# Kernel optimization log

Measured on AMD Instinct MI355X. Metric: run time of the kernel, lower is better.

Reference implementation:

```python
import math
import jax, jax.numpy as jnp
import numpy as np

N_HEAD = 16

def setup_inputs() -> dict:
    key = jax.random.key(0)
    ks = jax.random.split(key, 3)
    B, T, C = 2, 2048, 1024
    x = jax.random.normal(ks[0], (B, T, C), dtype=jnp.float32)
    W_attn = jax.random.normal(ks[1], (3 * C, C), dtype=jnp.float32) * (1.0 / math.sqrt(C))
    b_attn = jnp.zeros((3 * C,), dtype=jnp.float32)
    W_proj = jax.random.normal(ks[2], (C, C), dtype=jnp.float32) * (1.0 / math.sqrt(C))
    b_proj = jnp.zeros((C,), dtype=jnp.float32)
    return {"x": x, "W_attn": W_attn, "b_attn": b_attn, "W_proj": W_proj, "b_proj": b_proj}

def reference(x, W_attn, b_attn, W_proj, b_proj):
    B, T, C = x.shape
    H = N_HEAD
    Dh = C // H
    qkv = x @ W_attn.T + b_attn                      # [B,T,3C]
    q, k, v = jnp.split(qkv, 3, axis=-1)
    q = q.reshape(B, T, H, Dh).transpose(0, 2, 1, 3)  # [B,H,T,Dh]
    k = k.reshape(B, T, H, Dh).transpose(0, 2, 1, 3)
    v = v.reshape(B, T, H, Dh).transpose(0, 2, 1, 3)
    att = jnp.einsum('bhqd,bhkd->bhqk', q, k) * (1.0 / math.sqrt(Dh))
    # ALiBi-style RPE: bias[h, r, c] = -(r - c) * 2^(-8/H * (h+1)) for c <= r, 0 above diag
    rows = jnp.arange(T)[:, None]
    cols = jnp.arange(T)[None, :]
    dist = jnp.minimum((cols - rows).astype(jnp.float32), 0.0)  # [T,T]
    slopes = 2.0 ** (-8.0 / H * (jnp.arange(H, dtype=jnp.float32) + 1.0))  # [H]
    att = att + slopes[None, :, None, None] * dist[None, None]
    causal = cols <= rows                              # [T,T]
    att = jnp.where(causal[None, None], att, -jnp.inf)
    att = jax.nn.softmax(att, axis=-1)                 # dropout p=0.0 -> identity
    y = jnp.einsum('bhqk,bhkd->bhqd', att, v)          # [B,H,T,Dh]
    y = y.transpose(0, 2, 1, 3).reshape(B, T, C)
    y = y @ W_proj.T + b_proj
    return y
```

## Files before the change

kernel.cpp:

```cpp
#include <hip/hip_runtime.h>

typedef __bf16 bf16x8 __attribute__((ext_vector_type(8)));
typedef __bf16 bf16x4 __attribute__((ext_vector_type(4)));
typedef float  f32x4  __attribute__((ext_vector_type(4)));
typedef float  f32x16 __attribute__((ext_vector_type(16)));

#define TSEQ 2048
#define CDIM 1024
#define NHEAD 16
#define DH 64
#define SCALE2 0.1803368801111137f

__device__ __forceinline__ void gl_lds16(const void* g, void* l) {
  __builtin_amdgcn_global_load_lds(
      (const __attribute__((address_space(1))) unsigned int*)g,
      (__attribute__((address_space(3))) unsigned int*)l, 16, 0, 0);
}

__device__ __forceinline__ float fexp2(float x) { return __builtin_amdgcn_exp2f(x); }

__device__ __forceinline__ unsigned cvtpk(float a, float b) {
  unsigned r;
  asm("v_cvt_pk_bf16_f32 %0, %1, %2" : "=v"(r) : "v"(a), "v"(b));
  return r;
}
__device__ __forceinline__ void permswap(unsigned& x, unsigned& y) {
  asm("v_permlane32_swap_b32 %0, %1" : "+v"(x), "+v"(y));
}

__device__ __forceinline__ float tsum16(const f32x16& s) {
  float a0 = s[0] + s[1], a1 = s[2] + s[3], a2 = s[4] + s[5], a3 = s[6] + s[7];
  float a4 = s[8] + s[9], a5 = s[10] + s[11], a6 = s[12] + s[13], a7 = s[14] + s[15];
  float b0 = a0 + a1, b1 = a2 + a3, b2 = a4 + a5, b3 = a6 + a7;
  return (b0 + b1) + (b2 + b3);
}

__global__ __launch_bounds__(256) void cvt_bf16_all(
    const float* __restrict__ x, const float* __restrict__ wa,
    const float* __restrict__ wp, __bf16* __restrict__ xb,
    __bf16* __restrict__ wab, __bf16* __restrict__ wpb) {
  int i = blockIdx.x * 256 + threadIdx.x;
  const float* in;
  __bf16* out;
  int off;
  if (i < 524288)      { in = x;  out = xb;  off = i; }
  else if (i < 917504) { in = wa; out = wab; off = i - 524288; }
  else                 { in = wp; out = wpb; off = i - 917504; }
  const float4* p = (const float4*)(in + (size_t)off * 8);
  float4 a = p[0], b = p[1];
  bf16x8 r;
  r[0] = (__bf16)a.x; r[1] = (__bf16)a.y; r[2] = (__bf16)a.z; r[3] = (__bf16)a.w;
  r[4] = (__bf16)b.x; r[5] = (__bf16)b.y; r[6] = (__bf16)b.z; r[7] = (__bf16)b.w;
  *(bf16x8*)(out + (size_t)off * 8) = r;
}

__global__ __launch_bounds__(256) void gemm_qkv(
    const __bf16* __restrict__ A, const __bf16* __restrict__ Bw,
    const float* __restrict__ bias,
    __bf16* __restrict__ q_pack, __bf16* __restrict__ k_pack,
    __bf16* __restrict__ v_pack, int K) {
  __shared__ alignas(16) __bf16 lda[128 * 64];
  __shared__ alignas(16) __bf16 ldb[128 * 64];
  const int tid = threadIdx.x;
  const int lane = tid & 63, wid = tid >> 6;
  const int wm = wid >> 1, wn = wid & 1;
  const int hw = (int)(blockIdx.x + 24 * blockIdx.y);
  const int logi = (hw & 7) * 96 + (hw >> 3);
  const int row0 = (logi / 24) * 128, col0 = (logi % 24) * 128;
  f32x4 acc[4][4] = {};

  const int srow = lane >> 3;
  const int scb = ((lane & 7) ^ (lane >> 3)) * 16;

  for (int k0 = 0; k0 < K; k0 += 64) {
#pragma unroll
    for (int j = 0; j < 4; ++j) {
      int blk = j * 4 + wid;
      int r = blk * 8 + srow;
      char* la = (char*)lda + blk * 1024;
      char* lb = (char*)ldb + blk * 1024;
      gl_lds16((const char*)(A + (size_t)(row0 + r) * K + k0) + scb, la);
      gl_lds16((const char*)(Bw + (size_t)(col0 + r) * K + k0) + scb, lb);
    }
    __syncthreads();
#pragma unroll
    for (int kk = 0; kk < 2; ++kk) {
      const int sl = (((kk << 2) | (lane >> 4)) ^ (lane & 7)) * 16;
      bf16x8 af[4], bfr[4];
#pragma unroll
      for (int m = 0; m < 4; ++m)
        af[m] = *(const bf16x8*)((const char*)lda +
                                 (wm * 64 + m * 16 + (lane & 15)) * 128 + sl);
#pragma unroll
      for (int n = 0; n < 4; ++n)
        bfr[n] = *(const bf16x8*)((const char*)ldb +
                                  (wn * 64 + n * 16 + (lane & 15)) * 128 + sl);
#pragma unroll
      for (int m = 0; m < 4; ++m)
#pragma unroll
        for (int n = 0; n < 4; ++n)
          acc[m][n] = __builtin_amdgcn_mfma_f32_16x16x32_bf16(bfr[n], af[m], acc[m][n], 0, 0, 0);
    }
    __syncthreads();
  }
#pragma unroll
  for (int m = 0; m < 4; ++m) {
    const int r = row0 + wm * 64 + m * 16 + (lane & 15);
    const int bb = r >> 11, t = r & 2047;
    const size_t bhb = (size_t)bb * NHEAD;
#pragma unroll
    for (int n = 0; n < 4; ++n) {
      const int c0 = col0 + wn * 64 + n * 16 + (lane >> 4) * 4;
      const int sec = c0 >> 10;
      const int cc0 = c0 & 1023;
      const int hh = cc0 >> 6, d0 = cc0 & 63;
      const size_t bh = bhb + hh;
      const float4 bv = *(const float4*)&bias[c0];
      const float v0 = acc[m][n][0] + bv.x;
      const float v1 = acc[m][n][1] + bv.y;
      const float v2 = acc[m][n][2] + bv.z;
      const float v3 = acc[m][n][3] + bv.w;
      if (sec == 2) {
        const int j2 = t >> 5, kh = (t >> 4) & 1, half = d0 >> 5;
        const size_t base = (bh * 256 + (size_t)(j2 * 4 + kh * 2 + half)) * 512 + (size_t)(t & 7);
        const int l2v0 = (d0 & 31) + ((t >> 3) & 1) * 32;
        v_pack[base + (size_t)(l2v0 + 0) * 8] = (__bf16)v0;
        v_pack[base + (size_t)(l2v0 + 1) * 8] = (__bf16)v1;
        v_pack[base + (size_t)(l2v0 + 2) * 8] = (__bf16)v2;
        v_pack[base + (size_t)(l2v0 + 3) * 8] = (__bf16)v3;
      } else {
        const int ch = t >> 5, mm = d0 >> 4;
        const int l2 = (t & 31) + ((d0 >> 3) & 1) * 32, e0 = d0 & 7;
        const size_t idx = ((bh * 64 + ch) * 4 + (size_t)mm) * 512 + (size_t)l2 * 8 + e0;
        bf16x4 w;
        if (sec == 0) {
          w[0] = (__bf16)(v0 * SCALE2); w[1] = (__bf16)(v1 * SCALE2);
          w[2] = (__bf16)(v2 * SCALE2); w[3] = (__bf16)(v3 * SCALE2);
          *(bf16x4*)&q_pack[idx] = w;
        } else {
          w[0] = (__bf16)v0; w[1] = (__bf16)v1; w[2] = (__bf16)v2; w[3] = (__bf16)v3;
          *(bf16x4*)&k_pack[idx] = w;
        }
      }
    }
  }
}

__global__ __launch_bounds__(256) void gemm_proj(
    const __bf16* __restrict__ A, const __bf16* __restrict__ Bw,
    const float* __restrict__ bias, float* __restrict__ outf) {
  const int K = CDIM, N = CDIM;
  __shared__ alignas(16) __bf16 lda[64 * 64];
  __shared__ alignas(16) __bf16 ldb[128 * 64];
  const int tid = threadIdx.x;
  const int lane = tid & 63, wid = tid >> 6;
  const int hw = (int)(blockIdx.x + 8 * blockIdx.y);
  const int logi = (hw & 7) * 64 + (hw >> 3);
  const int row0 = (logi / 8) * 64, col0 = (logi % 8) * 128;
  f32x4 acc[4][2] = {};

  const int srow = lane >> 3;
  const int scb = ((lane & 7) ^ (lane >> 3)) * 16;

  for (int k0 = 0; k0 < K; k0 += 64) {
#pragma unroll
    for (int j = 0; j < 2; ++j) {
      int blk = j * 4 + wid;
      gl_lds16((const char*)(A + (size_t)(row0 + blk * 8 + srow) * K + k0) + scb,
               (char*)lda + blk * 1024);
    }
#pragma unroll
    for (int j = 0; j < 4; ++j) {
      int blk = j * 4 + wid;
      gl_lds16((const char*)(Bw + (size_t)(col0 + blk * 8 + srow) * K + k0) + scb,
               (char*)ldb + blk * 1024);
    }
    __syncthreads();
#pragma unroll
    for (int kk = 0; kk < 2; ++kk) {
      const int sl = (((kk << 2) | (lane >> 4)) ^ (lane & 7)) * 16;
      bf16x8 af[4], bfr[2];
#pragma unroll
      for (int m = 0; m < 4; ++m)
        af[m] = *(const bf16x8*)((const char*)lda + (m * 16 + (lane & 15)) * 128 + sl);
#pragma unroll
      for (int n = 0; n < 2; ++n)
        bfr[n] = *(const bf16x8*)((const char*)ldb +
                                  (wid * 32 + n * 16 + (lane & 15)) * 128 + sl);
#pragma unroll
      for (int m = 0; m < 4; ++m)
#pragma unroll
        for (int n = 0; n < 2; ++n)
          acc[m][n] = __builtin_amdgcn_mfma_f32_16x16x32_bf16(bfr[n], af[m], acc[m][n], 0, 0, 0);
    }
    __syncthreads();
  }
#pragma unroll
  for (int m = 0; m < 4; ++m) {
    const int r = row0 + m * 16 + (lane & 15);
#pragma unroll
    for (int n = 0; n < 2; ++n) {
      const int c0 = col0 + wid * 32 + n * 16 + (lane >> 4) * 4;
      const float4 bv = *(const float4*)&bias[c0];
      float4 o4;
      o4.x = acc[m][n][0] + bv.x;
      o4.y = acc[m][n][1] + bv.y;
      o4.z = acc[m][n][2] + bv.z;
      o4.w = acc[m][n][3] + bv.w;
      *(float4*)&outf[(size_t)r * N + c0] = o4;
    }
  }
}

__device__ __forceinline__ void softmax_pv(
    f32x16& s, bool domask, int lq, int hi,
    float& l_r, f32x16& o0, f32x16& o1,
    const bf16x8* va0, const bf16x8* va1) {
#pragma unroll
  for (int r = 0; r < 16; ++r) s[r] = fexp2(s[r]);
  if (domask) {
#pragma unroll
    for (int r = 0; r < 16; ++r) {
      int kof = (r & 3) + 8 * (r >> 2) + 4 * hi;
      if (kof > lq) s[r] = 0.f;
    }
  }
  l_r += tsum16(s);
  bf16x8 pb[2];
#pragma unroll
  for (int kh = 0; kh < 2; ++kh) {
    const int bq = kh * 8;
    unsigned w0 = cvtpk(s[bq + 0], s[bq + 1]);
    unsigned w1 = cvtpk(s[bq + 2], s[bq + 3]);
    unsigned w2 = cvtpk(s[bq + 4], s[bq + 5]);
    unsigned w3 = cvtpk(s[bq + 6], s[bq + 7]);
    permswap(w0, w2);
    permswap(w1, w3);
    union { unsigned u[4]; bf16x8 v; } pbu;
    pbu.u[0] = w0; pbu.u[1] = w1; pbu.u[2] = w2; pbu.u[3] = w3;
    pb[kh] = pbu.v;
  }
  o0 = __builtin_amdgcn_mfma_f32_32x32x16_bf16(va0[0], pb[0], o0, 0, 0, 0);
  o0 = __builtin_amdgcn_mfma_f32_32x32x16_bf16(va0[1], pb[1], o0, 0, 0, 0);
  o1 = __builtin_amdgcn_mfma_f32_32x32x16_bf16(va1[0], pb[0], o1, 0, 0, 0);
  o1 = __builtin_amdgcn_mfma_f32_32x32x16_bf16(va1[1], pb[1], o1, 0, 0, 0);
}

__global__ __launch_bounds__(64) void attn_fwd(
    const __bf16* __restrict__ q_pack, const __bf16* __restrict__ k_pack,
    const __bf16* __restrict__ v_pack, __bf16* __restrict__ y_buf) {
  const int lane = threadIdx.x;
  const int lq = lane & 31;
  const int hi = lane >> 5;
  const int bh = blockIdx.x;
  const int wv = blockIdx.y;
  const int b = bh >> 4, h = bh & 15;
  const int cH = 63 - wv, cL = wv;
  const float slope2 = exp2f(-0.5f * (float)(h + 1)) * 1.44269504f;
  const __bf16* qpk = q_pack + (size_t)bh * 64 * 2048;
  const __bf16* kpk = k_pack + (size_t)bh * 64 * 2048;
  const __bf16* vpk = v_pack + (size_t)bh * 64 * 2048;
  const int lo = lane * 8;

  bf16x8 qfH[4], qfL[4];
#pragma unroll
  for (int m = 0; m < 4; ++m) {
    qfH[m] = *(const bf16x8*)&qpk[(size_t)(cH * 4 + m) * 512 + lo];
    qfL[m] = *(const bf16x8*)&qpk[(size_t)(cL * 4 + m) * 512 + lo];
  }
  float pk_[16];
#pragma unroll
  for (int r = 0; r < 16; ++r)
    pk_[r] = slope2 * (float)((r & 3) + 8 * (r >> 2) + 4 * hi);

  f32x16 oH0 = {}, oH1 = {}, oL0 = {}, oL1 = {};
  float lH = 0.f, lL = 0.f;

  bf16x8 kf[4];
#pragma unroll
  for (int m = 0; m < 4; ++m)
    kf[m] = *(const bf16x8*)&kpk[(size_t)m * 512 + lo];

  for (int j = 0; j <= cH; ++j) {
    const int kt = j * 32;
    bf16x8 va0[2], va1[2];
#pragma unroll
    for (int kh = 0; kh < 2; ++kh) {
      va0[kh] = *(const bf16x8*)&vpk[(size_t)(j * 4 + kh * 2 + 0) * 512 + lo];
      va1[kh] = *(const bf16x8*)&vpk[(size_t)(j * 4 + kh * 2 + 1) * 512 + lo];
    }
    bf16x8 kn[4];
    const bool pre = (j < cH);
    if (pre) {
#pragma unroll
      for (int m = 0; m < 4; ++m)
        kn[m] = *(const bf16x8*)&kpk[(size_t)((j + 1) * 4 + m) * 512 + lo];
    }
    const float bH = slope2 * (float)(kt - cH * 32);
    f32x16 sH;
#pragma unroll
    for (int r = 0; r < 16; ++r) sH[r] = pk_[r] + bH;
#pragma unroll
    for (int m = 0; m < 4; ++m)
      sH = __builtin_amdgcn_mfma_f32_32x32x16_bf16(kf[m], qfH[m], sH, 0, 0, 0);
    const bool lact = (j <= cL);
    f32x16 sL;
    if (lact) {
      const float bL = slope2 * (float)(kt - cL * 32);
#pragma unroll
      for (int r = 0; r < 16; ++r) sL[r] = pk_[r] + bL;
#pragma unroll
      for (int m = 0; m < 4; ++m)
        sL = __builtin_amdgcn_mfma_f32_32x32x16_bf16(kf[m], qfL[m], sL, 0, 0, 0);
    }
    softmax_pv(sH, j == cH, lq, hi, lH, oH0, oH1, va0, va1);
    if (lact)
      softmax_pv(sL, j == cL, lq, hi, lL, oL0, oL1, va0, va1);
    if (pre) {
#pragma unroll
      for (int m = 0; m < 4; ++m) kf[m] = kn[m];
    }
  }
  lH += __shfl_xor(lH, 32, 64);
  lL += __shfl_xor(lL, 32, 64);

#pragma unroll
  for (int g2 = 0; g2 < 2; ++g2) {
    const int c = g2 ? cL : cH;
    const f32x16& a0 = g2 ? oL0 : oH0;
    const f32x16& a1 = g2 ? oL1 : oH1;
    const float inv = 1.0f / (g2 ? lL : lH);
    __bf16* yb = y_buf + ((size_t)b * TSEQ + c * 32 + lq) * CDIM + h * DH;
#pragma unroll
    for (int g = 0; g < 4; ++g) {
      bf16x4 v0, v1;
#pragma unroll
      for (int e = 0; e < 4; ++e) {
        v0[e] = (__bf16)(a0[4 * g + e] * inv);
        v1[e] = (__bf16)(a1[4 * g + e] * inv);
      }
      *(bf16x4*)&yb[8 * g + 4 * hi] = v0;
      *(bf16x4*)&yb[32 + 8 * g + 4 * hi] = v1;
    }
  }
}

extern "C" void kernel_launch(void* const* d_in, const int* in_sizes, int n_in,
                              void* d_out, int out_size, void* d_ws, size_t ws_size,
                              hipStream_t stream) {
  const float* x      = (const float*)d_in[0];
  const float* W_attn = (const float*)d_in[1];
  const float* b_attn = (const float*)d_in[2];
  const float* W_proj = (const float*)d_in[3];
  const float* b_proj = (const float*)d_in[4];
  float* out = (float*)d_out;
  char* ws = (char*)d_ws;
  const size_t MB = (size_t)1 << 20;
  __bf16* xb  = (__bf16*)(ws + 0 * MB);
  __bf16* wab = (__bf16*)(ws + 8 * MB);
  __bf16* wpb = (__bf16*)(ws + 14 * MB);
  __bf16* qpk = (__bf16*)(ws + 16 * MB);
  __bf16* kpk = (__bf16*)(ws + 24 * MB);
  __bf16* vpk = (__bf16*)(ws + 32 * MB);
  __bf16* yb  = (__bf16*)(ws + 40 * MB);

  cvt_bf16_all<<<4096, 256, 0, stream>>>(x, W_attn, W_proj, xb, wab, wpb);

  gemm_qkv<<<dim3(24, 32), 256, 0, stream>>>(xb, wab, b_attn, qpk, kpk, vpk, 1024);
  attn_fwd<<<dim3(32, 32), 64, 0, stream>>>(qpk, kpk, vpk, yb);
  gemm_proj<<<dim3(8, 64), 256, 0, stream>>>(yb, wpb, b_proj, out);
}
```

Baseline: 108.1 us.

## Shrink QKV GEMM tile to 64x128 and vectorize V-pack stores via swapped MFMA operands

The QKV projection GEMM now uses 64x128 tiles instead of 128x128, doubling the grid to 1536 blocks so more of the GPU's CUs are busy. Each wave covers a 64x32 slice. For the V section the MFMA operands are swapped so each lane holds four consecutive time steps, which lets the transposed V-pack write be one 4-wide bf16 store instead of four scalar stores. The trade-off is lower data reuse per block (B tile loaded more often relative to compute) and a branch on the section.

```diff
diff --git a/kernel.cpp b/kernel.cpp
--- a/kernel.cpp
+++ b/kernel.cpp
@@ -59,86 +59,115 @@
     const float* __restrict__ bias,
     __bf16* __restrict__ q_pack, __bf16* __restrict__ k_pack,
     __bf16* __restrict__ v_pack, int K) {
-  __shared__ alignas(16) __bf16 lda[128 * 64];
+  __shared__ alignas(16) __bf16 lda[64 * 64];
   __shared__ alignas(16) __bf16 ldb[128 * 64];
   const int tid = threadIdx.x;
   const int lane = tid & 63, wid = tid >> 6;
-  const int wm = wid >> 1, wn = wid & 1;
   const int hw = (int)(blockIdx.x + 24 * blockIdx.y);
-  const int logi = (hw & 7) * 96 + (hw >> 3);
-  const int row0 = (logi / 24) * 128, col0 = (logi % 24) * 128;
-  f32x4 acc[4][4] = {};
+  const int logi = (hw & 7) * 192 + (hw >> 3);
+  const int row0 = (logi / 24) * 64, col0 = (logi % 24) * 128;
+  const int sec = col0 >> 10;
+  const bool isV = (sec == 2);
+  f32x4 acc[4][2] = {};
 
   const int srow = lane >> 3;
   const int scb = ((lane & 7) ^ (lane >> 3)) * 16;
 
   for (int k0 = 0; k0 < K; k0 += 64) {
 #pragma unroll
+    for (int j = 0; j < 2; ++j) {
+      int blk = j * 4 + wid;
+      gl_lds16((const char*)(A + (size_t)(row0 + blk * 8 + srow) * K + k0) + scb,
+               (char*)lda + blk * 1024);
+    }
+#pragma unroll
     for (int j = 0; j < 4; ++j) {
       int blk = j * 4 + wid;
-      int r = blk * 8 + srow;
-      char* la = (char*)lda + blk * 1024;
-      char* lb = (char*)ldb + blk * 1024;
-      gl_lds16((const char*)(A + (size_t)(row0 + r) * K + k0) + scb, la);
-      gl_lds16((const char*)(Bw + (size_t)(col0 + r) * K + k0) + scb, lb);
+      gl_lds16((const char*)(Bw + (size_t)(col0 + blk * 8 + srow) * K + k0) + scb,
+               (char*)ldb + blk * 1024);
     }
     __syncthreads();
 #pragma unroll
     for (int kk = 0; kk < 2; ++kk) {
       const int sl = (((kk << 2) | (lane >> 4)) ^ (lane & 7)) * 16;
-      bf16x8 af[4], bfr[4];
+      bf16x8 af[4], bfr[2];
 #pragma unroll
       for (int m = 0; m < 4; ++m)
-        af[m] = *(const bf16x8*)((const char*)lda +
-                                 (wm * 64 + m * 16 + (lane & 15)) * 128 + sl);
-#pragma unroll
-      for (int n = 0; n < 4; ++n)
+        af[m] = *(const bf16x8*)((const char*)lda + (m * 16 + (lane & 15)) * 128 + sl);
+#pragma unroll
+      for (int n = 0; n < 2; ++n)
         bfr[n] = *(const bf16x8*)((const char*)ldb +
-                                  (wn * 64 + n * 16 + (lane & 15)) * 128 + sl);
-#pragma unroll
-      for (int m = 0; m < 4; ++m)
-#pragma unroll
-        for (int n = 0; n < 4; ++n)
-          acc[m][n] = __builtin_amdgcn_mfma_f32_16x16x32_bf16(bfr[n], af[m], acc[m][n], 0, 0, 0);
+                                  (wid * 32 + n * 16 + (lane & 15)) * 128 + sl);
+      if (isV) {
+#pragma unroll
+        for (int m = 0; m < 4; ++m)
+#pragma unroll
+          for (int n = 0; n < 2; ++n)
+            acc[m][n] = __builtin_amdgcn_mfma_f32_16x16x32_bf16(af[m], bfr[n], acc[m][n], 0, 0, 0);
+      } else {
+#pragma unroll
+        for (int m = 0; m < 4; ++m)
+#pragma unroll
+          for (int n = 0; n < 2; ++n)
+            acc[m][n] = __builtin_amdgcn_mfma_f32_16x16x32_bf16(bfr[n], af[m], acc[m][n], 0, 0, 0);
+      }
     }
     __syncthreads();
   }
-#pragma unroll
-  for (int m = 0; m < 4; ++m) {
-    const int r = row0 + wm * 64 + m * 16 + (lane & 15);
-    const int bb = r >> 11, t = r & 2047;
-    const size_t bhb = (size_t)bb * NHEAD;
-#pragma unroll
-    for (int n = 0; n < 4; ++n) {
-      const int c0 = col0 + wn * 64 + n * 16 + (lane >> 4) * 4;
-      const int sec = c0 >> 10;
-      const int cc0 = c0 & 1023;
-      const int hh = cc0 >> 6, d0 = cc0 & 63;
-      const size_t bh = bhb + hh;
-      const float4 bv = *(const float4*)&bias[c0];
-      const float v0 = acc[m][n][0] + bv.x;
-      const float v1 = acc[m][n][1] + bv.y;
-      const float v2 = acc[m][n][2] + bv.z;
-      const float v3 = acc[m][n][3] + bv.w;
-      if (sec == 2) {
-        const int j2 = t >> 5, kh = (t >> 4) & 1, half = d0 >> 5;
-        const size_t base = (bh * 256 + (size_t)(j2 * 4 + kh * 2 + half)) * 512 + (size_t)(t & 7);
-        const int l2v0 = (d0 & 31) + ((t >> 3) & 1) * 32;
-        v_pack[base + (size_t)(l2v0 + 0) * 8] = (__bf16)v0;
-        v_pack[base + (size_t)(l2v0 + 1) * 8] = (__bf16)v1;
-        v_pack[base + (size_t)(l2v0 + 2) * 8] = (__bf16)v2;
-        v_pack[base + (size_t)(l2v0 + 3) * 8] = (__bf16)v3;
-      } else {
+
+  if (isV) {
+#pragma unroll
+    for (int m = 0; m < 4; ++m) {
+      const int t0g = row0 + m * 16 + (lane >> 4) * 4;
+      const int bb = t0g >> 11, t0 = t0g & 2047;
+      const size_t bhb = (size_t)bb * NHEAD;
+#pragma unroll
+      for (int n = 0; n < 2; ++n) {
+        const int c = col0 + wid * 32 + n * 16 + (lane & 15);
+        const int cc = c & 1023;
+        const int hh = cc >> 6, d = cc & 63;
+        const size_t bh = bhb + hh;
+        const float bvs = bias[c];
+        const int j2 = t0 >> 5, kh = (t0 >> 4) & 1, half = d >> 5;
+        const int l2v = (d & 31) + ((t0 >> 3) & 1) * 32;
+        const size_t idx = (bh * 256 + (size_t)(j2 * 4 + kh * 2 + half)) * 512 +
+                           (size_t)l2v * 8 + (t0 & 7);
+        bf16x4 w;
+        w[0] = (__bf16)(acc[m][n][0] + bvs);
+        w[1] = (__bf16)(acc[m][n][1] + bvs);
+        w[2] = (__bf16)(acc[m][n][2] + bvs);
+        w[3] = (__bf16)(acc[m][n][3] + bvs);
+        *(bf16x4*)&v_pack[idx] = w;
+      }
+    }
+  } else {
+#pragma unroll
+    for (int m = 0; m < 4; ++m) {
+      const int r = row0 + m * 16 + (lane & 15);
+      const int bb = r >> 11, t = r & 2047;
+      const size_t bhb = (size_t)bb * NHEAD;
+#pragma unroll
+      for (int n = 0; n < 2; ++n) {
+        const int c0 = col0 + wid * 32 + n * 16 + (lane >> 4) * 4;
+        const int cc0 = c0 & 1023;
+        const int hh = cc0 >> 6, d0 = cc0 & 63;
+        const size_t bh = bhb + hh;
+        const float4 bv = *(const float4*)&bias[c0];
         const int ch = t >> 5, mm = d0 >> 4;
         const int l2 = (t & 31) + ((d0 >> 3) & 1) * 32, e0 = d0 & 7;
         const size_t idx = ((bh * 64 + ch) * 4 + (size_t)mm) * 512 + (size_t)l2 * 8 + e0;
         bf16x4 w;
         if (sec == 0) {
-          w[0] = (__bf16)(v0 * SCALE2); w[1] = (__bf16)(v1 * SCALE2);
-          w[2] = (__bf16)(v2 * SCALE2); w[3] = (__bf16)(v3 * SCALE2);
+          w[0] = (__bf16)((acc[m][n][0] + bv.x) * SCALE2);
+          w[1] = (__bf16)((acc[m][n][1] + bv.y) * SCALE2);
+          w[2] = (__bf16)((acc[m][n][2] + bv.z) * SCALE2);
+          w[3] = (__bf16)((acc[m][n][3] + bv.w) * SCALE2);
           *(bf16x4*)&q_pack[idx] = w;
         } else {
-          w[0] = (__bf16)v0; w[1] = (__bf16)v1; w[2] = (__bf16)v2; w[3] = (__bf16)v3;
+          w[0] = (__bf16)(acc[m][n][0] + bv.x);
+          w[1] = (__bf16)(acc[m][n][1] + bv.y);
+          w[2] = (__bf16)(acc[m][n][2] + bv.z);
+          w[3] = (__bf16)(acc[m][n][3] + bv.w);
           *(bf16x4*)&k_pack[idx] = w;
         }
       }
@@ -366,7 +395,7 @@
 
   cvt_bf16_all<<<4096, 256, 0, stream>>>(x, W_attn, W_proj, xb, wab, wpb);
 
-  gemm_qkv<<<dim3(24, 32), 256, 0, stream>>>(xb, wab, b_attn, qpk, kpk, vpk, 1024);
+  gemm_qkv<<<dim3(24, 64), 256, 0, stream>>>(xb, wab, b_attn, qpk, kpk, vpk, 1024);
   attn_fwd<<<dim3(32, 32), 64, 0, stream>>>(qpk, kpk, vpk, yb);
   gemm_proj<<<dim3(8, 64), 256, 0, stream>>>(yb, wpb, b_proj, out);
 }
```

Result: slower. 113.8 us (+5.3%).
